# Performance work log

Measured on AMD Instinct MI355X. Metric: run time of the kernel, lower is better.

## Reference

```python
import jax, jax.numpy as jnp
import numpy as np

N = 50000
E = 800000
IN_C = 256
OUT_C = 256
HEADS = 8
HEAD_C = OUT_C // HEADS  # 32
BNECK = OUT_C // 4       # 64
NEG_SLOPE = 0.2
BN_EPS = 1e-5


def _bn(x, gamma, beta):
    # BatchNorm1d over node dim, batch statistics (deterministic train-mode math)
    mu = jnp.mean(x, axis=0)
    var = jnp.var(x, axis=0)
    return (x - mu) * jax.lax.rsqrt(var + BN_EPS) * gamma + beta


def setup_inputs() -> dict:
    key = jax.random.key(0)
    ks = jax.random.split(key, 16)
    s = lambda fan: 1.0 / np.sqrt(fan)
    x = jax.random.normal(ks[0], (N, IN_C), dtype=jnp.float32)
    edge_index = jax.random.randint(ks[1], (2, E), 0, N, dtype=jnp.int64)
    return {
        "x": x,
        "edge_index": edge_index,
        # GATConv params (lin has no bias in PyG)
        "W_lin": jax.random.normal(ks[2], (IN_C, HEADS * HEAD_C), jnp.float32) * s(IN_C),
        "att_src": jax.random.normal(ks[3], (HEADS, HEAD_C), jnp.float32) * s(HEAD_C),
        "att_dst": jax.random.normal(ks[4], (HEADS, HEAD_C), jnp.float32) * s(HEAD_C),
        "conv_bias": jnp.zeros((HEADS * HEAD_C,), jnp.float32),
        "W_res": jax.random.normal(ks[5], (IN_C, HEADS * HEAD_C), jnp.float32) * s(IN_C),
        # gnn.BatchNorm
        "g_norm": jnp.ones((OUT_C,), jnp.float32),
        "b_norm": jnp.zeros((OUT_C,), jnp.float32),
        # Bottleneck down
        "W_down": jax.random.normal(ks[6], (OUT_C, BNECK), jnp.float32) * s(OUT_C),
        "b_down": jnp.zeros((BNECK,), jnp.float32),
        "g_down": jnp.ones((BNECK,), jnp.float32),
        "bb_down": jnp.zeros((BNECK,), jnp.float32),
        # Bottleneck up
        "W_up": jax.random.normal(ks[7], (BNECK, OUT_C), jnp.float32) * s(BNECK),
        "b_up": jnp.zeros((OUT_C,), jnp.float32),
        "g_up": jnp.ones((OUT_C,), jnp.float32),
        "bb_up": jnp.zeros((OUT_C,), jnp.float32),
    }


def _forward(x, edge_index, W_lin, att_src, att_dst, conv_bias, W_res,
             g_norm, b_norm, W_down, b_down, g_down, bb_down,
             W_up, b_up, g_up, bb_up):
    src, dst = edge_index[0], edge_index[1]
    # --- GATConv ---
    xh = (x @ W_lin).reshape(N, HEADS, HEAD_C)            # [N,H,C]
    a_src = jnp.einsum("nhc,hc->nh", xh, att_src)          # [N,H]
    a_dst = jnp.einsum("nhc,hc->nh", xh, att_dst)          # [N,H]
    e = a_src[src] + a_dst[dst]                             # [E,H]
    e = jnp.where(e > 0, e, NEG_SLOPE * e)                  # leaky_relu
    # segment softmax over destination nodes (numerically stable)
    m = jax.ops.segment_max(e, dst, num_segments=N)         # [N,H]
    m = jnp.where(jnp.isfinite(m), m, 0.0)
    ex = jnp.exp(e - m[dst])
    denom = jax.ops.segment_sum(ex, dst, num_segments=N)    # [N,H]
    alpha = ex / (denom[dst] + 1e-16)                        # [E,H]
    msgs = xh[src] * alpha[:, :, None]                       # [E,H,C]
    out = jax.ops.segment_sum(msgs, dst, num_segments=N)    # [N,H,C]
    out = out.reshape(N, HEADS * HEAD_C) + conv_bias + x @ W_res  # GAT residual + bias
    # --- norm + act ---
    h = jax.nn.elu(_bn(out, g_norm, b_norm))
    # --- bottleneck ---
    d = jax.nn.elu(_bn(h @ W_down + b_down, g_down, bb_down))
    u = jax.nn.elu(_bn(d @ W_up + b_up, g_up, bb_up))
    h = h + u
    # dropout: eval mode (identity); in==out so identity skip
    return h + x


def reference(x, edge_index, W_lin, att_src, att_dst, conv_bias, W_res,
              g_norm, b_norm, W_down, b_down, g_down, bb_down,
              W_up, b_up, g_up, bb_up):
    return _forward(x, edge_index, W_lin, att_src, att_dst, conv_bias, W_res,
                    g_norm, b_norm, W_down, b_down, g_down, bb_down,
                    W_up, b_up, g_up, bb_up)
```

## Files before the change

kernel.cpp:

```cpp
#include <hip/hip_runtime.h>

#define NN 50000
#define EE 800000
#define HEADS 8
#define NEG 0.2f
#define BN_EPS 1e-5f
#define SCAN_B 196

typedef unsigned int uint;
typedef unsigned short ushort;

typedef __bf16 bf16x8 __attribute__((ext_vector_type(8)));
typedef float f32x4 __attribute__((ext_vector_type(4)));

__device__ __forceinline__ float bflo(uint u) { return __uint_as_float(u << 16); }
__device__ __forceinline__ float bfhi(uint u) { return __uint_as_float(u & 0xffff0000u); }
__device__ __forceinline__ float bf1(ushort u) { return __uint_as_float(((uint)u) << 16); }
__device__ __forceinline__ ushort f2bf(float f) {
  uint u = __float_as_uint(f);
  u += 0x7fff + ((u >> 16) & 1);
  return (ushort)(u >> 16);
}
__device__ __forceinline__ float eluf(float v) { return v > 0.f ? v : expm1f(v); }

__global__ void k_detect(const uint* __restrict__ xw, const int* __restrict__ ew,
                         int* __restrict__ flags) {
  int l = threadIdx.x;
  int good = 0, zeros = 0;
#pragma unroll
  for (int j = 0; j < 4; ++j) {
    uint lo = xw[l * 4 + j] & 0xffffu;
    uint ex = (lo >> 7) & 0xffu;
    good += (ex >= 110u && ex <= 140u) ? 1 : 0;
    zeros += (ew[2 * (l * 4 + j) + 1] == 0) ? 1 : 0;
  }
  for (int o = 32; o; o >>= 1) { good += __shfl_down(good, o); zeros += __shfl_down(zeros, o); }
  if (l == 0) { flags[0] = (good >= 128) ? 1 : 0; flags[1] = (zeros >= 200) ? 1 : 0; }
}

__global__ void k_params(const void* p0, const void* p1, const void* p2, const void* p3,
                         const void* p4, const void* p5, const void* p6, const void* p7,
                         const void* p8, const void* p9, const void* p10,
                         float* __restrict__ P, const int* __restrict__ flags) {
  const void* srcs[11] = {p0, p1, p2, p3, p4, p5, p6, p7, p8, p9, p10};
  const int sz[11]  = {256, 256, 256, 256, 256, 64, 64, 64, 256, 256, 256};
  const int off[11] = {0, 256, 512, 768, 1024, 1280, 1344, 1408, 1472, 1728, 1984};
  int b = blockIdx.x, t = threadIdx.x;
  if (t < sz[b]) {
    const void* s = srcs[b];
    float v = flags[0] ? bf1(((const ushort*)s)[t]) : ((const float*)s)[t];
    P[off[b] + t] = v;
  }
}

__global__ void k_transpose(const void* __restrict__ src, ushort* __restrict__ dst,
                            int R, int C, int D, const int* __restrict__ flags) {
  __shared__ ushort tile[64][65];
  int r0 = blockIdx.x * 64, c0 = blockIdx.y * 64;
  int t = threadIdx.x;
  int tr = t >> 6;
  int tc = t & 63;
  int bf = flags[0];
#pragma unroll
  for (int i = 0; i < 16; ++i) {
    int rl = tr + i * 4;
    int r = r0 + rl, c = c0 + tc;
    float v = 0.f;
    if (r < R && c < C)
      v = bf ? bf1(((const ushort*)src)[(size_t)r * C + c])
             : ((const float*)src)[(size_t)r * C + c];
    tile[rl][tc] = f2bf(v);
  }
  __syncthreads();
#pragma unroll
  for (int i = 0; i < 16; ++i) {
    int cl = tr + i * 4;
    int rl = tc;
    int c = c0 + cl, r = r0 + rl;
    if (c < D && r < R)
      dst[(size_t)c * R + r] = (c < C) ? tile[rl][cl] : (ushort)0;
  }
}

__global__ void k_cast(const void* __restrict__ x, ushort* __restrict__ xb,
                       const int* __restrict__ flags) {
  size_t base = ((size_t)blockIdx.x * 256 + threadIdx.x) * 8;
  if (base >= (size_t)NN * 256) return;
  if (flags[0]) {
    *(uint4*)(xb + base) = *(const uint4*)((const ushort*)x + base);
  } else {
    const float* xf = (const float*)x;
    float4 a = *(const float4*)(xf + base);
    float4 b = *(const float4*)(xf + base + 4);
    uint4 o;
    o.x = (uint)f2bf(a.x) | ((uint)f2bf(a.y) << 16);
    o.y = (uint)f2bf(a.z) | ((uint)f2bf(a.w) << 16);
    o.z = (uint)f2bf(b.x) | ((uint)f2bf(b.y) << 16);
    o.w = (uint)f2bf(b.z) | ((uint)f2bf(b.w) << 16);
    *(uint4*)(xb + base) = o;
  }
}

__global__ void k_edges(const int* __restrict__ raw, int* __restrict__ sc, int* __restrict__ dc,
                        int* __restrict__ count, const int* __restrict__ flags) {
  int e = blockIdx.x * 256 + threadIdx.x;
  if (e >= EE) return;
  int s, d;
  if (flags[1]) { s = raw[2 * e]; d = raw[2 * (EE + e)]; }
  else          { s = raw[e];     d = raw[EE + e]; }
  if ((uint)s >= NN) s = 0;
  if ((uint)d >= NN) d = 0;
  sc[e] = s; dc[e] = d;
  atomicAdd(&count[d], 1);
}

__global__ __launch_bounds__(256)
void k_gemm(const ushort* __restrict__ A, const ushort* __restrict__ Bt,
            int M, int K, int mode,
            ushort* __restrict__ o_xh, ushort* __restrict__ o_xres,
            float* __restrict__ o_f32, int NC, const float* __restrict__ bias) {
  __shared__ __align__(16) ushort As[128 * 32];
  __shared__ __align__(16) ushort Bs[128 * 32];
  int t = threadIdx.x;
  int l = t & 63, w = t >> 6;
  int wr = w >> 1, wc = w & 1;
  int lr = l & 15, lq = l >> 4;
  int m0 = blockIdx.y * 128;
  int n0 = blockIdx.x * 128;

  f32x4 acc[4][4];
#pragma unroll
  for (int i = 0; i < 4; ++i)
#pragma unroll
    for (int j = 0; j < 4; ++j) acc[i][j] = (f32x4){0.f, 0.f, 0.f, 0.f};

  for (int kt = 0; kt < K; kt += 32) {
    __syncthreads();
#pragma unroll
    for (int r = 0; r < 2; ++r) {
      int ci = r * 256 + t;
      int m = ci >> 2, ko = (ci & 3) << 3;
      int gm = m0 + m; gm = gm < M ? gm : M - 1;
      *(uint4*)(&As[m * 32 + ko]) = *(const uint4*)(A + (size_t)gm * K + kt + ko);
      *(uint4*)(&Bs[m * 32 + ko]) = *(const uint4*)(Bt + (size_t)(n0 + m) * K + kt + ko);
    }
    __syncthreads();
    bf16x8 af[4], bf[4];
#pragma unroll
    for (int i = 0; i < 4; ++i) {
      af[i] = *(const bf16x8*)(&As[(wr * 64 + i * 16 + lr) * 32 + lq * 8]);
      bf[i] = *(const bf16x8*)(&Bs[(wc * 64 + i * 16 + lr) * 32 + lq * 8]);
    }
#pragma unroll
    for (int i = 0; i < 4; ++i)
#pragma unroll
      for (int j = 0; j < 4; ++j)
        acc[i][j] = __builtin_amdgcn_mfma_f32_16x16x32_bf16(af[i], bf[j], acc[i][j], 0, 0, 0);
  }

#pragma unroll
  for (int i = 0; i < 4; ++i) {
    int gr0 = m0 + wr * 64 + i * 16 + lq * 4;
#pragma unroll
    for (int j = 0; j < 4; ++j) {
      int gc = n0 + wc * 64 + j * 16 + lr;
#pragma unroll
      for (int r = 0; r < 4; ++r) {
        int row = gr0 + r;
        if (row >= M) continue;
        float v = acc[i][j][r];
        if (mode == 0) {
          if (gc < 256) o_xh[(size_t)row * 256 + gc] = f2bf(v);
          else          o_xres[(size_t)row * 256 + (gc - 256)] = f2bf(v);
        } else {
          if (gc < NC) o_f32[(size_t)row * NC + gc] = v + bias[gc];
        }
      }
    }
  }
}

__global__ void k_attn(const ushort* __restrict__ xh, const float* __restrict__ P,
                       float* __restrict__ a_src, float* __restrict__ a_dst) {
  int id = blockIdx.x * 256 + threadIdx.x;
  if (id >= NN * HEADS) return;
  int n = id >> 3, h = id & 7;
  const uint4* xr = (const uint4*)(xh + (size_t)n * 256 + h * 32);
  const float4* pa = (const float4*)(P + h * 32);
  const float4* pd = (const float4*)(P + 256 + h * 32);
  float s = 0.f, d = 0.f;
#pragma unroll
  for (int j = 0; j < 4; ++j) {
    uint4 q = xr[j];
    float4 a0 = pa[2 * j], a1 = pa[2 * j + 1];
    float4 d0 = pd[2 * j], d1 = pd[2 * j + 1];
    float x0 = bflo(q.x), x1 = bfhi(q.x), x2 = bflo(q.y), x3 = bfhi(q.y);
    float x4 = bflo(q.z), x5 = bfhi(q.z), x6 = bflo(q.w), x7 = bfhi(q.w);
    s += x0 * a0.x + x1 * a0.y + x2 * a0.z + x3 * a0.w
       + x4 * a1.x + x5 * a1.y + x6 * a1.z + x7 * a1.w;
    d += x0 * d0.x + x1 * d0.y + x2 * d0.z + x3 * d0.w
       + x4 * d1.x + x5 * d1.y + x6 * d1.z + x7 * d1.w;
  }
  a_src[id] = s; a_dst[id] = d;
}

__global__ void k_scan_bs(const int* __restrict__ count, int* __restrict__ bsum) {
  __shared__ int s[256];
  int i = blockIdx.x * 256 + threadIdx.x;
  s[threadIdx.x] = (i < NN) ? count[i] : 0;
  __syncthreads();
  for (int off = 128; off > 0; off >>= 1) {
    if (threadIdx.x < off) s[threadIdx.x] += s[threadIdx.x + off];
    __syncthreads();
  }
  if (threadIdx.x == 0) bsum[blockIdx.x] = s[0];
}

__global__ void k_scan_top(const int* __restrict__ bsum, int* __restrict__ boff,
                           int* __restrict__ rowptr) {
  __shared__ int s[256];
  int t = threadIdx.x;
  int v = (t < SCAN_B) ? bsum[t] : 0;
  s[t] = v;
  __syncthreads();
  for (int off = 1; off < 256; off <<= 1) {
    int u = (t >= off) ? s[t - off] : 0;
    __syncthreads();
    s[t] += u;
    __syncthreads();
  }
  boff[t] = s[t] - v;
  if (t == 255) rowptr[NN] = s[255];
}

__global__ void k_scan_wr(const int* __restrict__ count, const int* __restrict__ boff,
                          int* __restrict__ rowptr, int* __restrict__ rowwork) {
  __shared__ int s[256];
  int b = blockIdx.x, t = threadIdx.x;
  int i = b * 256 + t;
  int v = (i < NN) ? count[i] : 0;
  s[t] = v;
  __syncthreads();
  for (int off = 1; off < 256; off <<= 1) {
    int u = (t >= off) ? s[t - off] : 0;
    __syncthreads();
    s[t] += u;
    __syncthreads();
  }
  if (i < NN) {
    int ex = boff[b] + s[t] - v;
    rowptr[i] = ex;
    rowwork[i] = ex;
  }
}

__global__ void k_scatter(const int* __restrict__ sc, const int* __restrict__ dc,
                          int* __restrict__ rowwork, int* __restrict__ perm_src) {
  int e = blockIdx.x * 256 + threadIdx.x;
  if (e >= EE) return;
  int pos = atomicAdd(&rowwork[dc[e]], 1);
  perm_src[pos] = sc[e];
}

__global__ __launch_bounds__(256)
void k_aggregate(const int* __restrict__ rowptr, const int* __restrict__ perm_src,
                 const float* __restrict__ a_src, const float* __restrict__ a_dst,
                 const ushort* __restrict__ xh, const ushort* __restrict__ xres,
                 const float* __restrict__ bias, float* __restrict__ out) {
  int n = blockIdx.x * 4 + (threadIdx.x >> 6);
  int l = threadIdx.x & 63;
  if (n >= NN) return;
  int half = l >> 5;
  int q = l & 31;
  int h = q >> 2;
  float ad = a_dst[n * 8 + h];
  int st = rowptr[n], en = rowptr[n + 1];
  float a0 = 0.f, a1 = 0.f, a2 = 0.f, a3 = 0.f;
  float a4 = 0.f, a5 = 0.f, a6 = 0.f, a7 = 0.f, sum = 0.f;
#pragma unroll 2
  for (int p = st + half; p < en; p += 2) {
    int s = perm_src[p];
    float v = a_src[s * 8 + h] + ad;
    v = v > 0.f ? v : NEG * v;
    float wgt = __expf(fminf(v, 60.f));
    sum += wgt;
    uint4 t4 = *(const uint4*)(xh + (size_t)s * 256 + q * 8);
    a0 += wgt * bflo(t4.x); a1 += wgt * bfhi(t4.x);
    a2 += wgt * bflo(t4.y); a3 += wgt * bfhi(t4.y);
    a4 += wgt * bflo(t4.z); a5 += wgt * bfhi(t4.z);
    a6 += wgt * bflo(t4.w); a7 += wgt * bfhi(t4.w);
  }
  sum += __shfl_xor(sum, 32);
  a0 += __shfl_xor(a0, 32); a1 += __shfl_xor(a1, 32);
  a2 += __shfl_xor(a2, 32); a3 += __shfl_xor(a3, 32);
  a4 += __shfl_xor(a4, 32); a5 += __shfl_xor(a5, 32);
  a6 += __shfl_xor(a6, 32); a7 += __shfl_xor(a7, 32);
  if (half == 0) {
    float inv = 1.0f / (sum + 1e-16f);
    int cb = q * 8;
    float4 b0 = *(const float4*)(bias + cb);
    float4 b1 = *(const float4*)(bias + cb + 4);
    uint4 qr = *(const uint4*)(xres + (size_t)n * 256 + cb);
    float4 o0, o1;
    o0.x = a0 * inv + b0.x + bflo(qr.x);
    o0.y = a1 * inv + b0.y + bfhi(qr.x);
    o0.z = a2 * inv + b0.z + bflo(qr.y);
    o0.w = a3 * inv + b0.w + bfhi(qr.y);
    o1.x = a4 * inv + b1.x + bflo(qr.z);
    o1.y = a5 * inv + b1.y + bfhi(qr.z);
    o1.z = a6 * inv + b1.z + bflo(qr.w);
    o1.w = a7 * inv + b1.w + bfhi(qr.w);
    *(float4*)(out + (size_t)n * 256 + cb) = o0;
    *(float4*)(out + (size_t)n * 256 + cb + 4) = o1;
  }
}

__global__ void k_stats(const float* __restrict__ x, float* __restrict__ sums, int n, int C) {
  int t = threadIdx.x;
  int c = t & (C - 1);
  int rl = t / C;
  int rpb = 256 / C;
  int rows = (n + gridDim.x - 1) / gridDim.x;
  int r0 = blockIdx.x * rows;
  int r1 = r0 + rows; if (r1 > n) r1 = n;
  float s = 0.f, ss = 0.f;
  for (int r = r0 + rl; r < r1; r += rpb) {
    float v = x[(size_t)r * C + c];
    s += v; ss += v * v;
  }
  atomicAdd(&sums[c], s);
  atomicAdd(&sums[C + c], ss);
}

__global__ void k_bnact1(const float* __restrict__ xin, const float* __restrict__ sums,
                         const float* __restrict__ g, const float* __restrict__ b,
                         ushort* __restrict__ h1b) {
  int id = blockIdx.x * 256 + threadIdx.x;
  size_t base = (size_t)id * 4;
  if (base >= (size_t)NN * 256) return;
  int c = (int)(base & 255);
  const float invN = 1.0f / NN;
  float4 sm = *(const float4*)(sums + c);
  float4 sq = *(const float4*)(sums + 256 + c);
  float4 g4 = *(const float4*)(g + c);
  float4 b4 = *(const float4*)(b + c);
  float4 v = *(const float4*)(xin + base);
  float vv[4] = {v.x, v.y, v.z, v.w};
  float smv[4] = {sm.x, sm.y, sm.z, sm.w}, sqv[4] = {sq.x, sq.y, sq.z, sq.w};
  float gv[4] = {g4.x, g4.y, g4.z, g4.w}, bv[4] = {b4.x, b4.y, b4.z, b4.w};
  float o[4];
#pragma unroll
  for (int j = 0; j < 4; ++j) {
    float mean = smv[j] * invN;
    float var = sqv[j] * invN - mean * mean;
    float sc = gv[j] * rsqrtf(var + BN_EPS);
    o[j] = eluf((vv[j] - mean) * sc + bv[j]);
  }
  uint2 pk;
  pk.x = (uint)f2bf(o[0]) | ((uint)f2bf(o[1]) << 16);
  pk.y = (uint)f2bf(o[2]) | ((uint)f2bf(o[3]) << 16);
  *(uint2*)(h1b + base) = pk;
}

__global__ void k_bnact2(const float* __restrict__ xin, const float* __restrict__ sums,
                         const float* __restrict__ g, const float* __restrict__ b,
                         ushort* __restrict__ db) {
  int id = blockIdx.x * 256 + threadIdx.x;
  size_t base = (size_t)id * 4;
  if (base >= (size_t)NN * 64) return;
  int c = (int)(base & 63);
  const float invN = 1.0f / NN;
  float4 sm = *(const float4*)(sums + c);
  float4 sq = *(const float4*)(sums + 64 + c);
  float4 g4 = *(const float4*)(g + c);
  float4 b4 = *(const float4*)(b + c);
  float4 v = *(const float4*)(xin + base);
  float vv[4] = {v.x, v.y, v.z, v.w};
  float smv[4] = {sm.x, sm.y, sm.z, sm.w}, sqv[4] = {sq.x, sq.y, sq.z, sq.w};
  float gv[4] = {g4.x, g4.y, g4.z, g4.w}, bv[4] = {b4.x, b4.y, b4.z, b4.w};
  float o[4];
#pragma unroll
  for (int j = 0; j < 4; ++j) {
    float mean = smv[j] * invN;
    float var = sqv[j] * invN - mean * mean;
    float sc = gv[j] * rsqrtf(var + BN_EPS);
    o[j] = eluf((vv[j] - mean) * sc + bv[j]);
  }
  uint2 pk;
  pk.x = (uint)f2bf(o[0]) | ((uint)f2bf(o[1]) << 16);
  pk.y = (uint)f2bf(o[2]) | ((uint)f2bf(o[3]) << 16);
  *(uint2*)(db + base) = pk;
}

__global__ void k_final(const float* __restrict__ upre, const float* __restrict__ sums,
                        const float* __restrict__ g, const float* __restrict__ b,
                        const ushort* __restrict__ h1b, const void* __restrict__ xsrc,
                        void* __restrict__ outv, const int* __restrict__ flags) {
  int id = blockIdx.x * 256 + threadIdx.x;
  size_t base = (size_t)id * 4;
  if (base >= (size_t)NN * 256) return;
  int c = (int)(base & 255);
  const float invN = 1.0f / NN;
  float4 sm = *(const float4*)(sums + c);
  float4 sq = *(const float4*)(sums + 256 + c);
  float4 g4 = *(const float4*)(g + c);
  float4 b4 = *(const float4*)(b + c);
  float4 v = *(const float4*)(upre + base);
  uint2 qh = *(const uint2*)(h1b + base);
  float xv[4];
  if (flags[0]) {
    uint2 qx = *(const uint2*)((const ushort*)xsrc + base);
    xv[0] = bflo(qx.x); xv[1] = bfhi(qx.x); xv[2] = bflo(qx.y); xv[3] = bfhi(qx.y);
  } else {
    float4 qx = *(const float4*)((const float*)xsrc + base);
    xv[0] = qx.x; xv[1] = qx.y; xv[2] = qx.z; xv[3] = qx.w;
  }
  float vv[4] = {v.x, v.y, v.z, v.w};
  float hv[4] = {bflo(qh.x), bfhi(qh.x), bflo(qh.y), bfhi(qh.y)};
  float smv[4] = {sm.x, sm.y, sm.z, sm.w}, sqv[4] = {sq.x, sq.y, sq.z, sq.w};
  float gv[4] = {g4.x, g4.y, g4.z, g4.w}, bv[4] = {b4.x, b4.y, b4.z, b4.w};
  float o[4];
#pragma unroll
  for (int j = 0; j < 4; ++j) {
    float mean = smv[j] * invN;
    float var = sqv[j] * invN - mean * mean;
    float sc = gv[j] * rsqrtf(var + BN_EPS);
    o[j] = eluf((vv[j] - mean) * sc + bv[j]) + hv[j] + xv[j];
  }
  if (flags[0]) {
    uint2 pk;
    pk.x = (uint)f2bf(o[0]) | ((uint)f2bf(o[1]) << 16);
    pk.y = (uint)f2bf(o[2]) | ((uint)f2bf(o[3]) << 16);
    *(uint2*)((ushort*)outv + base) = pk;
  } else {
    *(float4*)((float*)outv + base) = make_float4(o[0], o[1], o[2], o[3]);
  }
}

extern "C" void kernel_launch(void* const* d_in, const int* in_sizes, int n_in,
                              void* d_out, int out_size, void* d_ws, size_t ws_size,
                              hipStream_t stream) {
  const void* x      = d_in[0];
  const int*  ei     = (const int*)d_in[1];
  const void* W_lin  = d_in[2];
  const void* att_s  = d_in[3];
  const void* att_d  = d_in[4];
  const void* c_bias = d_in[5];
  const void* W_res  = d_in[6];
  const void* g_norm = d_in[7];
  const void* b_norm = d_in[8];
  const void* W_down = d_in[9];
  const void* b_down = d_in[10];
  const void* g_down = d_in[11];
  const void* bb_down= d_in[12];
  const void* W_up   = d_in[13];
  const void* b_up   = d_in[14];
  const void* g_up   = d_in[15];
  const void* bb_up  = d_in[16];

  char* ws = (char*)d_ws;
  size_t off = 0;
  auto alloc = [&](size_t bytes) -> char* {
    char* p = ws + off;
    off = (off + bytes + 255) & ~(size_t)255;
    return p;
  };
  int*   flags  = (int*)alloc(2 * 4);
  int*   count  = (int*)alloc((size_t)NN * 4);
  float* sums1  = (float*)alloc(512 * 4);
  float* sums2  = (float*)alloc(128 * 4);
  float* sums3  = (float*)alloc(512 * 4);
  size_t zbytes = off;
  float* P      = (float*)alloc(2240 * 4);
  int* bsum     = (int*)alloc(256 * 4);
  int* boff     = (int*)alloc(256 * 4);
  int* rowptr   = (int*)alloc((size_t)(NN + 1) * 4);
  int* rowwork  = (int*)alloc((size_t)(NN + 1) * 4);
  int* src_c    = (int*)alloc((size_t)EE * 4);
  int* dst_c    = (int*)alloc((size_t)EE * 4);
  int* perm_src = (int*)alloc((size_t)EE * 4);
  ushort* bt1   = (ushort*)alloc((size_t)512 * 256 * 2);
  ushort* bt2   = (ushort*)alloc((size_t)128 * 256 * 2);
  ushort* bt3   = (ushort*)alloc((size_t)256 * 64 * 2);
  float* a_src  = (float*)alloc((size_t)NN * 8 * 4);
  float* a_dst  = (float*)alloc((size_t)NN * 8 * 4);
  ushort* x_bf  = (ushort*)alloc((size_t)NN * 256 * 2);
  ushort* xh    = (ushort*)alloc((size_t)NN * 256 * 2);
  ushort* xres  = (ushort*)alloc((size_t)NN * 256 * 2);
  float* out_gat= (float*)alloc((size_t)NN * 256 * 4);
  ushort* d_b   = (ushort*)alloc((size_t)NN * 64 * 2);
  ushort* h1b  = x_bf;
  float*  d_pre = (float*)xres;
  float*  u_pre = out_gat;

  hipMemsetAsync(d_ws, 0, zbytes, stream);

  hipLaunchKernelGGL(k_detect, dim3(1), dim3(64), 0, stream, (const uint*)x, ei, flags);
  hipLaunchKernelGGL(k_params, dim3(11), dim3(256), 0, stream,
                     att_s, att_d, c_bias, g_norm, b_norm, b_down, g_down, bb_down,
                     b_up, g_up, bb_up, P, flags);
  hipLaunchKernelGGL(k_transpose, dim3(4, 4), dim3(256), 0, stream, W_lin, bt1, 256, 256, 256, flags);
  hipLaunchKernelGGL(k_transpose, dim3(4, 4), dim3(256), 0, stream, W_res, bt1 + 256 * 256, 256, 256, 256, flags);
  hipLaunchKernelGGL(k_transpose, dim3(4, 2), dim3(256), 0, stream, W_down, bt2, 256, 64, 128, flags);
  hipLaunchKernelGGL(k_transpose, dim3(1, 4), dim3(256), 0, stream, W_up, bt3, 64, 256, 256, flags);
  hipLaunchKernelGGL(k_cast, dim3(6250), dim3(256), 0, stream, x, x_bf, flags);
  hipLaunchKernelGGL(k_edges, dim3((EE + 255) / 256), dim3(256), 0, stream,
                     ei, src_c, dst_c, count, flags);

  hipLaunchKernelGGL(k_gemm, dim3(4, 391), dim3(256), 0, stream, x_bf, bt1, NN, 256, 0,
                     xh, xres, (float*)nullptr, 0, (const float*)nullptr);
  hipLaunchKernelGGL(k_attn, dim3((NN * 8 + 255) / 256), dim3(256), 0, stream,
                     xh, P, a_src, a_dst);

  hipLaunchKernelGGL(k_scan_bs, dim3(SCAN_B), dim3(256), 0, stream, count, bsum);
  hipLaunchKernelGGL(k_scan_top, dim3(1), dim3(256), 0, stream, bsum, boff, rowptr);
  hipLaunchKernelGGL(k_scan_wr, dim3(SCAN_B), dim3(256), 0, stream, count, boff, rowptr, rowwork);
  hipLaunchKernelGGL(k_scatter, dim3((EE + 255) / 256), dim3(256), 0, stream,
                     src_c, dst_c, rowwork, perm_src);

  hipLaunchKernelGGL(k_aggregate, dim3(NN / 4), dim3(256), 0, stream, rowptr, perm_src,
                     a_src, a_dst, xh, xres, P + 512, out_gat);

  hipLaunchKernelGGL(k_stats, dim3(256), dim3(256), 0, stream, out_gat, sums1, NN, 256);
  hipLaunchKernelGGL(k_bnact1, dim3(NN * 256 / 4 / 256), dim3(256), 0, stream,
                     out_gat, sums1, P + 768, P + 1024, h1b);

  hipLaunchKernelGGL(k_gemm, dim3(1, 391), dim3(256), 0, stream, h1b, bt2, NN, 256, 1,
                     (ushort*)nullptr, (ushort*)nullptr, d_pre, 64, P + 1280);
  hipLaunchKernelGGL(k_stats, dim3(256), dim3(256), 0, stream, d_pre, sums2, NN, 64);
  hipLaunchKernelGGL(k_bnact2, dim3(NN * 64 / 4 / 256), dim3(256), 0, stream,
                     d_pre, sums2, P + 1344, P + 1408, d_b);

  hipLaunchKernelGGL(k_gemm, dim3(2, 391), dim3(256), 0, stream, d_b, bt3, NN, 64, 2,
                     (ushort*)nullptr, (ushort*)nullptr, u_pre, 256, P + 1472);
  hipLaunchKernelGGL(k_stats, dim3(256), dim3(256), 0, stream, u_pre, sums3, NN, 256);
  hipLaunchKernelGGL(k_final, dim3(NN * 256 / 4 / 256), dim3(256), 0, stream,
                     u_pre, sums3, P + 1728, P + 1984, h1b, x, d_out, flags);
}
```

Before: 613.8 us.

## Fuse input cast into GEMM, store intermediates as bf16, prefetch in aggregate

Removes the separate fp32-to-bf16 cast kernel of x by converting inside the first GEMM's A-tile load. Stores the GAT output and the bottleneck pre-activations as bf16 instead of fp32, roughly halving traffic for the stats, BN/activation and GEMM epilogue passes. Adds software prefetching of the next edge's source index, logit and features in the aggregation loop. This costs precision in the intermediates that feed the batch statistics, and buffer aliasing changes.

Result: slower. 735.6 us (+19.8%).

```diff
diff --git a/kernel.cpp b/kernel.cpp
--- a/kernel.cpp
+++ b/kernel.cpp
@@ -20,6 +20,9 @@
   uint u = __float_as_uint(f);
   u += 0x7fff + ((u >> 16) & 1);
   return (ushort)(u >> 16);
+}
+__device__ __forceinline__ uint pk2(float a, float b) {
+  return (uint)f2bf(a) | ((uint)f2bf(b) << 16);
 }
 __device__ __forceinline__ float eluf(float v) { return v > 0.f ? v : expm1f(v); }
 
@@ -82,25 +85,6 @@
   }
 }
 
-__global__ void k_cast(const void* __restrict__ x, ushort* __restrict__ xb,
-                       const int* __restrict__ flags) {
-  size_t base = ((size_t)blockIdx.x * 256 + threadIdx.x) * 8;
-  if (base >= (size_t)NN * 256) return;
-  if (flags[0]) {
-    *(uint4*)(xb + base) = *(const uint4*)((const ushort*)x + base);
-  } else {
-    const float* xf = (const float*)x;
-    float4 a = *(const float4*)(xf + base);
-    float4 b = *(const float4*)(xf + base + 4);
-    uint4 o;
-    o.x = (uint)f2bf(a.x) | ((uint)f2bf(a.y) << 16);
-    o.y = (uint)f2bf(a.z) | ((uint)f2bf(a.w) << 16);
-    o.z = (uint)f2bf(b.x) | ((uint)f2bf(b.y) << 16);
-    o.w = (uint)f2bf(b.z) | ((uint)f2bf(b.w) << 16);
-    *(uint4*)(xb + base) = o;
-  }
-}
-
 __global__ void k_edges(const int* __restrict__ raw, int* __restrict__ sc, int* __restrict__ dc,
                         int* __restrict__ count, const int* __restrict__ flags) {
   int e = blockIdx.x * 256 + threadIdx.x;
@@ -115,10 +99,11 @@
 }
 
 __global__ __launch_bounds__(256)
-void k_gemm(const ushort* __restrict__ A, const ushort* __restrict__ Bt,
+void k_gemm(const void* __restrict__ A, const ushort* __restrict__ Bt,
+            const int* __restrict__ flags, int aMode,
             int M, int K, int mode,
             ushort* __restrict__ o_xh, ushort* __restrict__ o_xres,
-            float* __restrict__ o_f32, int NC, const float* __restrict__ bias) {
+            ushort* __restrict__ o_bf, int NC, const float* __restrict__ bias) {
   __shared__ __align__(16) ushort As[128 * 32];
   __shared__ __align__(16) ushort Bs[128 * 32];
   int t = threadIdx.x;
@@ -127,6 +112,9 @@
   int lr = l & 15, lq = l >> 4;
   int m0 = blockIdx.y * 128;
   int n0 = blockIdx.x * 128;
+  const int af32 = (aMode == 1) && (flags[0] == 0);
+  const ushort* Ab = (const ushort*)A;
+  const float*  Af = (const float*)A;
 
   f32x4 acc[4][4];
 #pragma unroll
@@ -141,7 +129,16 @@
       int ci = r * 256 + t;
       int m = ci >> 2, ko = (ci & 3) << 3;
       int gm = m0 + m; gm = gm < M ? gm : M - 1;
-      *(uint4*)(&As[m * 32 + ko]) = *(const uint4*)(A + (size_t)gm * K + kt + ko);
+      if (af32) {
+        float4 u0 = *(const float4*)(Af + (size_t)gm * K + kt + ko);
+        float4 u1 = *(const float4*)(Af + (size_t)gm * K + kt + ko + 4);
+        uint4 o;
+        o.x = pk2(u0.x, u0.y); o.y = pk2(u0.z, u0.w);
+        o.z = pk2(u1.x, u1.y); o.w = pk2(u1.z, u1.w);
+        *(uint4*)(&As[m * 32 + ko]) = o;
+      } else {
+        *(uint4*)(&As[m * 32 + ko]) = *(const uint4*)(Ab + (size_t)gm * K + kt + ko);
+      }
       *(uint4*)(&Bs[m * 32 + ko]) = *(const uint4*)(Bt + (size_t)(n0 + m) * K + kt + ko);
     }
     __syncthreads();
@@ -173,7 +170,7 @@
           if (gc < 256) o_xh[(size_t)row * 256 + gc] = f2bf(v);
           else          o_xres[(size_t)row * 256 + (gc - 256)] = f2bf(v);
         } else {
-          if (gc < NC) o_f32[(size_t)row * NC + gc] = v + bias[gc];
+          if (gc < NC) o_bf[(size_t)row * NC + gc] = f2bf(v + bias[gc]);
         }
       }
     }
@@ -266,7 +263,7 @@
 void k_aggregate(const int* __restrict__ rowptr, const int* __restrict__ perm_src,
                  const float* __restrict__ a_src, const float* __restrict__ a_dst,
                  const ushort* __restrict__ xh, const ushort* __restrict__ xres,
-                 const float* __restrict__ bias, float* __restrict__ out) {
+                 const float* __restrict__ bias, ushort* __restrict__ outb) {
   int n = blockIdx.x * 4 + (threadIdx.x >> 6);
   int l = threadIdx.x & 63;
   if (n >= NN) return;
@@ -277,18 +274,30 @@
   int st = rowptr[n], en = rowptr[n + 1];
   float a0 = 0.f, a1 = 0.f, a2 = 0.f, a3 = 0.f;
   float a4 = 0.f, a5 = 0.f, a6 = 0.f, a7 = 0.f, sum = 0.f;
-#pragma unroll 2
-  for (int p = st + half; p < en; p += 2) {
-    int s = perm_src[p];
-    float v = a_src[s * 8 + h] + ad;
+  int p = st + half;
+  int s_c = 0; float e_c = 0.f; uint4 x_c = {0, 0, 0, 0};
+  if (p < en) {
+    s_c = perm_src[p];
+    e_c = a_src[s_c * 8 + h];
+    x_c = *(const uint4*)(xh + (size_t)s_c * 256 + q * 8);
+  }
+  for (; p < en; p += 2) {
+    int pn = p + 2;
+    int s_n = 0; float e_n = 0.f; uint4 x_n = {0, 0, 0, 0};
+    if (pn < en) {
+      s_n = perm_src[pn];
+      e_n = a_src[s_n * 8 + h];
+      x_n = *(const uint4*)(xh + (size_t)s_n * 256 + q * 8);
+    }
+    float v = e_c + ad;
     v = v > 0.f ? v : NEG * v;
     float wgt = __expf(fminf(v, 60.f));
     sum += wgt;
-    uint4 t4 = *(const uint4*)(xh + (size_t)s * 256 + q * 8);
-    a0 += wgt * bflo(t4.x); a1 += wgt * bfhi(t4.x);
-    a2 += wgt * bflo(t4.y); a3 += wgt * bfhi(t4.y);
-    a4 += wgt * bflo(t4.z); a5 += wgt * bfhi(t4.z);
-    a6 += wgt * bflo(t4.w); a7 += wgt * bfhi(t4.w);
+    a0 += wgt * bflo(x_c.x); a1 += wgt * bfhi(x_c.x);
+    a2 += wgt * bflo(x_c.y); a3 += wgt * bfhi(x_c.y);
+    a4 += wgt * bflo(x_c.z); a5 += wgt * bfhi(x_c.z);
+    a6 += wgt * bflo(x_c.w); a7 += wgt * bfhi(x_c.w);
+    s_c = s_n; e_c = e_n; x_c = x_n;
   }
   sum += __shfl_xor(sum, 32);
   a0 += __shfl_xor(a0, 32); a1 += __shfl_xor(a1, 32);
@@ -301,38 +310,39 @@
     float4 b0 = *(const float4*)(bias + cb);
     float4 b1 = *(const float4*)(bias + cb + 4);
     uint4 qr = *(const uint4*)(xres + (size_t)n * 256 + cb);
-    float4 o0, o1;
-    o0.x = a0 * inv + b0.x + bflo(qr.x);
-    o0.y = a1 * inv + b0.y + bfhi(qr.x);
-    o0.z = a2 * inv + b0.z + bflo(qr.y);
-    o0.w = a3 * inv + b0.w + bfhi(qr.y);
-    o1.x = a4 * inv + b1.x + bflo(qr.z);
-    o1.y = a5 * inv + b1.y + bfhi(qr.z);
-    o1.z = a6 * inv + b1.z + bflo(qr.w);
-    o1.w = a7 * inv + b1.w + bfhi(qr.w);
-    *(float4*)(out + (size_t)n * 256 + cb) = o0;
-    *(float4*)(out + (size_t)n * 256 + cb + 4) = o1;
-  }
-}
-
-__global__ void k_stats(const float* __restrict__ x, float* __restrict__ sums, int n, int C) {
+    uint4 pk;
+    pk.x = pk2(a0 * inv + b0.x + bflo(qr.x), a1 * inv + b0.y + bfhi(qr.x));
+    pk.y = pk2(a2 * inv + b0.z + bflo(qr.y), a3 * inv + b0.w + bfhi(qr.y));
+    pk.z = pk2(a4 * inv + b1.x + bflo(qr.z), a5 * inv + b1.y + bfhi(qr.z));
+    pk.w = pk2(a6 * inv + b1.z + bflo(qr.w), a7 * inv + b1.w + bfhi(qr.w));
+    *(uint4*)(outb + (size_t)n * 256 + cb) = pk;
+  }
+}
+
+__global__ void k_stats_bf(const ushort* __restrict__ x, float* __restrict__ sums, int n, int C) {
   int t = threadIdx.x;
-  int c = t & (C - 1);
-  int rl = t / C;
-  int rpb = 256 / C;
+  int half = C >> 1;
+  int c2 = t & (half - 1);
+  int rl = t / half;
+  int rpb = 256 / half;
   int rows = (n + gridDim.x - 1) / gridDim.x;
   int r0 = blockIdx.x * rows;
   int r1 = r0 + rows; if (r1 > n) r1 = n;
-  float s = 0.f, ss = 0.f;
+  const uint* xu = (const uint*)x;
+  float s0 = 0.f, ss0 = 0.f, s1 = 0.f, ss1 = 0.f;
   for (int r = r0 + rl; r < r1; r += rpb) {
-    float v = x[(size_t)r * C + c];
-    s += v; ss += v * v;
-  }
-  atomicAdd(&sums[c], s);
-  atomicAdd(&sums[C + c], ss);
-}
-
-__global__ void k_bnact1(const float* __restrict__ xin, const float* __restrict__ sums,
+    uint qv = xu[(size_t)r * half + c2];
+    float v0 = bflo(qv), v1 = bfhi(qv);
+    s0 += v0; ss0 += v0 * v0;
+    s1 += v1; ss1 += v1 * v1;
+  }
+  atomicAdd(&sums[2 * c2], s0);
+  atomicAdd(&sums[2 * c2 + 1], s1);
+  atomicAdd(&sums[C + 2 * c2], ss0);
+  atomicAdd(&sums[C + 2 * c2 + 1], ss1);
+}
+
+__global__ void k_bnact1(const ushort* __restrict__ xin, const float* __restrict__ sums,
                          const float* __restrict__ g, const float* __restrict__ b,
                          ushort* __restrict__ h1b) {
   int id = blockIdx.x * 256 + threadIdx.x;
@@ -344,8 +354,8 @@
   float4 sq = *(const float4*)(sums + 256 + c);
   float4 g4 = *(const float4*)(g + c);
   float4 b4 = *(const float4*)(b + c);
-  float4 v = *(const float4*)(xin + base);
-  float vv[4] = {v.x, v.y, v.z, v.w};
+  uint2 qv = *(const uint2*)(xin + base);
+  float vv[4] = {bflo(qv.x), bfhi(qv.x), bflo(qv.y), bfhi(qv.y)};
   float smv[4] = {sm.x, sm.y, sm.z, sm.w}, sqv[4] = {sq.x, sq.y, sq.z, sq.w};
   float gv[4] = {g4.x, g4.y, g4.z, g4.w}, bv[4] = {b4.x, b4.y, b4.z, b4.w};
   float o[4];
@@ -357,12 +367,12 @@
     o[j] = eluf((vv[j] - mean) * sc + bv[j]);
   }
   uint2 pk;
-  pk.x = (uint)f2bf(o[0]) | ((uint)f2bf(o[1]) << 16);
-  pk.y = (uint)f2bf(o[2]) | ((uint)f2bf(o[3]) << 16);
+  pk.x = pk2(o[0], o[1]);
+  pk.y = pk2(o[2], o[3]);
   *(uint2*)(h1b + base) = pk;
 }
 
-__global__ void k_bnact2(const float* __restrict__ xin, const float* __restrict__ sums,
+__global__ void k_bnact2(const ushort* __restrict__ xin, const float* __restrict__ sums,
                          const float* __restrict__ g, const float* __restrict__ b,
                          ushort* __restrict__ db) {
   int id = blockIdx.x * 256 + threadIdx.x;
@@ -374,8 +384,8 @@
   float4 sq = *(const float4*)(sums + 64 + c);
   float4 g4 = *(const float4*)(g + c);
   float4 b4 = *(const float4*)(b + c);
-  float4 v = *(const float4*)(xin + base);
-  float vv[4] = {v.x, v.y, v.z, v.w};
+  uint2 qv = *(const uint2*)(xin + base);
+  float vv[4] = {bflo(qv.x), bfhi(qv.x), bflo(qv.y), bfhi(qv.y)};
   float smv[4] = {sm.x, sm.y, sm.z, sm.w}, sqv[4] = {sq.x, sq.y, sq.z, sq.w};
   float gv[4] = {g4.x, g4.y, g4.z, g4.w}, bv[4] = {b4.x, b4.y, b4.z, b4.w};
   float o[4];
@@ -387,12 +397,12 @@
     o[j] = eluf((vv[j] - mean) * sc + bv[j]);
   }
   uint2 pk;
-  pk.x = (uint)f2bf(o[0]) | ((uint)f2bf(o[1]) << 16);
-  pk.y = (uint)f2bf(o[2]) | ((uint)f2bf(o[3]) << 16);
+  pk.x = pk2(o[0], o[1]);
+  pk.y = pk2(o[2], o[3]);
   *(uint2*)(db + base) = pk;
 }
 
-__global__ void k_final(const float* __restrict__ upre, const float* __restrict__ sums,
+__global__ void k_final(const ushort* __restrict__ upre, const float* __restrict__ sums,
                         const float* __restrict__ g, const float* __restrict__ b,
                         const ushort* __restrict__ h1b, const void* __restrict__ xsrc,
                         void* __restrict__ outv, const int* __restrict__ flags) {
@@ -405,7 +415,7 @@
   float4 sq = *(const float4*)(sums + 256 + c);
   float4 g4 = *(const float4*)(g + c);
   float4 b4 = *(const float4*)(b + c);
-  float4 v = *(const float4*)(upre + base);
+  uint2 qv = *(const uint2*)(upre + base);
   uint2 qh = *(const uint2*)(h1b + base);
   float xv[4];
   if (flags[0]) {
@@ -415,7 +425,7 @@
     float4 qx = *(const float4*)((const float*)xsrc + base);
     xv[0] = qx.x; xv[1] = qx.y; xv[2] = qx.z; xv[3] = qx.w;
   }
-  float vv[4] = {v.x, v.y, v.z, v.w};
+  float vv[4] = {bflo(qv.x), bfhi(qv.x), bflo(qv.y), bfhi(qv.y)};
   float hv[4] = {bflo(qh.x), bfhi(qh.x), bflo(qh.y), bfhi(qh.y)};
   float smv[4] = {sm.x, sm.y, sm.z, sm.w}, sqv[4] = {sq.x, sq.y, sq.z, sq.w};
   float gv[4] = {g4.x, g4.y, g4.z, g4.w}, bv[4] = {b4.x, b4.y, b4.z, b4.w};
@@ -429,8 +439,8 @@
   }
   if (flags[0]) {
     uint2 pk;
-    pk.x = (uint)f2bf(o[0]) | ((uint)f2bf(o[1]) << 16);
-    pk.y = (uint)f2bf(o[2]) | ((uint)f2bf(o[3]) << 16);
+    pk.x = pk2(o[0], o[1]);
+    pk.y = pk2(o[2], o[3]);
     *(uint2*)((ushort*)outv + base) = pk;
   } else {
     *(float4*)((float*)outv + base) = make_float4(o[0], o[1], o[2], o[3]);
@@ -484,14 +494,13 @@
   ushort* bt3   = (ushort*)alloc((size_t)256 * 64 * 2);
   float* a_src  = (float*)alloc((size_t)NN * 8 * 4);
   float* a_dst  = (float*)alloc((size_t)NN * 8 * 4);
-  ushort* x_bf  = (ushort*)alloc((size_t)NN * 256 * 2);
   ushort* xh    = (ushort*)alloc((size_t)NN * 256 * 2);
   ushort* xres  = (ushort*)alloc((size_t)NN * 256 * 2);
-  float* out_gat= (float*)alloc((size_t)NN * 256 * 4);
+  ushort* og_b  = (ushort*)alloc((size_t)NN * 256 * 2);
   ushort* d_b   = (ushort*)alloc((size_t)NN * 64 * 2);
-  ushort* h1b  = x_bf;
-  float*  d_pre = (float*)xres;
-  float*  u_pre = out_gat;
+  ushort* h1b    = xres;
+  ushort* d_pre_b= xh;
+  ushort* u_pre_b= og_b;
 
   hipMemsetAsync(d_ws, 0, zbytes, stream);
 
@@ -503,12 +512,11 @@
   hipLaunchKernelGGL(k_transpose, dim3(4, 4), dim3(256), 0, stream, W_res, bt1 + 256 * 256, 256, 256, 256, flags);
   hipLaunchKernelGGL(k_transpose, dim3(4, 2), dim3(256), 0, stream, W_down, bt2, 256, 64, 128, flags);
   hipLaunchKernelGGL(k_transpose, dim3(1, 4), dim3(256), 0, stream, W_up, bt3, 64, 256, 256, flags);
-  hipLaunchKernelGGL(k_cast, dim3(6250), dim3(256), 0, stream, x, x_bf, flags);
   hipLaunchKernelGGL(k_edges, dim3((EE + 255) / 256), dim3(256), 0, stream,
                      ei, src_c, dst_c, count, flags);
 
-  hipLaunchKernelGGL(k_gemm, dim3(4, 391), dim3(256), 0, stream, x_bf, bt1, NN, 256, 0,
-                     xh, xres, (float*)nullptr, 0, (const float*)nullptr);
+  hipLaunchKernelGGL(k_gemm, dim3(4, 391), dim3(256), 0, stream, x, bt1, flags, 1,
+                     NN, 256, 0, xh, xres, (ushort*)nullptr, 0, (const float*)nullptr);
   hipLaunchKernelGGL(k_attn, dim3((NN * 8 + 255) / 256), dim3(256), 0, stream,
                      xh, P, a_src, a_dst);
 
@@ -519,21 +527,21 @@
                      src_c, dst_c, rowwork, perm_src);
 
   hipLaunchKernelGGL(k_aggregate, dim3(NN / 4), dim3(256), 0, stream, rowptr, perm_src,
-                     a_src, a_dst, xh, xres, P + 512, out_gat);
-
-  hipLaunchKernelGGL(k_stats, dim3(256), dim3(256), 0, stream, out_gat, sums1, NN, 256);
+                     a_src, a_dst, xh, xres, P + 512, og_b);
+
+  hipLaunchKernelGGL(k_stats_bf, dim3(256), dim3(256), 0, stream, og_b, sums1, NN, 256);
   hipLaunchKernelGGL(k_bnact1, dim3(NN * 256 / 4 / 256), dim3(256), 0, stream,
-                     out_gat, sums1, P + 768, P + 1024, h1b);
-
-  hipLaunchKernelGGL(k_gemm, dim3(1, 391), dim3(256), 0, stream, h1b, bt2, NN, 256, 1,
-                     (ushort*)nullptr, (ushort*)nullptr, d_pre, 64, P + 1280);
-  hipLaunchKernelGGL(k_stats, dim3(256), dim3(256), 0, stream, d_pre, sums2, NN, 64);
+                     og_b, sums1, P + 768, P + 1024, h1b);
+
+  hipLaunchKernelGGL(k_gemm, dim3(1, 391), dim3(256), 0, stream, h1b, bt2, flags, 0,
+                     NN, 256, 1, (ushort*)nullptr, (ushort*)nullptr, d_pre_b, 64, P + 1280);
+  hipLaunchKernelGGL(k_stats_bf, dim3(256), dim3(256), 0, stream, d_pre_b, sums2, NN, 64);
   hipLaunchKernelGGL(k_bnact2, dim3(NN * 64 / 4 / 256), dim3(256), 0, stream,
-                     d_pre, sums2, P + 1344, P + 1408, d_b);
-
-  hipLaunchKernelGGL(k_gemm, dim3(2, 391), dim3(256), 0, stream, d_b, bt3, NN, 64, 2,
-                     (ushort*)nullptr, (ushort*)nullptr, u_pre, 256, P + 1472);
-  hipLaunchKernelGGL(k_stats, dim3(256), dim3(256), 0, stream, u_pre, sums3, NN, 256);
+                     d_pre_b, sums2, P + 1344, P + 1408, d_b);
+
+  hipLaunchKernelGGL(k_gemm, dim3(2, 391), dim3(256), 0, stream, d_b, bt3, flags, 0,
+                     NN, 64, 1, (ushort*)nullptr, (ushort*)nullptr, u_pre_b, 256, P + 1472);
+  hipLaunchKernelGGL(k_stats_bf, dim3(256), dim3(256), 0, stream, u_pre_b, sums3, NN, 256);
   hipLaunchKernelGGL(k_final, dim3(NN * 256 / 4 / 256), dim3(256), 0, stream,
-                     u_pre, sums3, P + 1728, P + 1984, h1b, x, d_out, flags);
-}
+                     u_pre_b, sums3, P + 1728, P + 1984, h1b, x, d_out, flags);
+}
```
